# Optimization experiments

Measured on AMD Instinct MI355X. Metric: run time of the kernel, lower is better.

The kernel has to match this reference:

```python
import jax, jax.numpy as jnp
import numpy as np

N = 100000      # nodes
E = 1600000     # edges
D = 128         # hidden_dim
H = 8           # num_heads
DH = D // H     # per-head dim (out_dim in MultiHeadAttentionLayer)
EPS = 1e-5


def layer_norm(x, g, b):
    mu = jnp.mean(x, axis=-1, keepdims=True)
    var = jnp.var(x, axis=-1, keepdims=True)
    return (x - mu) * jax.lax.rsqrt(var + EPS) * g + b


def setup_inputs() -> dict:
    key = jax.random.key(0)
    ks = jax.random.split(key, 16)
    s = 1.0 / np.sqrt(D)
    inp = {
        "h": jax.random.normal(ks[0], (N, D), jnp.float32),
        "src": jax.random.randint(ks[1], (E,), 0, N, jnp.int32),
        "dst": jax.random.randint(ks[2], (E,), 0, N, jnp.int32),
        # attention projections (use_bias=False)
        "Wq": jax.random.uniform(ks[3], (D, D), jnp.float32, -s, s),
        "Wk": jax.random.uniform(ks[4], (D, D), jnp.float32, -s, s),
        "Wv": jax.random.uniform(ks[5], (D, D), jnp.float32, -s, s),
        # output projection O (bias=True)
        "Wo": jax.random.uniform(ks[6], (D, D), jnp.float32, -s, s),
        "bo": jnp.zeros((D,), jnp.float32),
        # layer norms
        "g1": jnp.ones((D,), jnp.float32),
        "b1": jnp.zeros((D,), jnp.float32),
        "g2": jnp.ones((D,), jnp.float32),
        "b2": jnp.zeros((D,), jnp.float32),
        # FFN
        "W1": jax.random.uniform(ks[7], (D, 2 * D), jnp.float32, -s, s),
        "c1": jnp.zeros((2 * D,), jnp.float32),
        "W2": jax.random.uniform(ks[8], (2 * D, D), jnp.float32, -1.0 / np.sqrt(2 * D), 1.0 / np.sqrt(2 * D)),
        "c2": jnp.zeros((D,), jnp.float32),
    }
    return inp


def reference(h, src, dst, Wq, Wk, Wv, Wo, bo, g1, b1, g2, b2, W1, c1, W2, c2):
    n = h.shape[0]
    Q = (h @ Wq).reshape(n, H, DH)
    K = (h @ Wk).reshape(n, H, DH)
    V = (h @ Wv).reshape(n, H, DH)

    # per-edge score: (K[src] * Q[dst]).sum(-1), scaled exp with clamp
    score = jnp.einsum('ehd,ehd->eh', K[src], Q[dst])          # [E, H]
    score = jnp.exp(jnp.clip(score / np.sqrt(DH), -5.0, 5.0))  # [E, H]

    # scatter-sum aggregation into destination nodes
    wV = jax.ops.segment_sum(V[src] * score[:, :, None], dst, num_segments=n)  # [N, H, DH]
    z = jax.ops.segment_sum(score, dst, num_segments=n)                        # [N, H]

    # possible_empty=True: divide only where z > 0
    zb = z[:, :, None]
    head_out = jnp.where(zb > 0, wV / jnp.where(zb > 0, zb, 1.0), wV)

    a = head_out.reshape(n, D) @ Wo + bo
    hh = layer_norm(h + a, g1, b1)
    ff = jax.nn.relu(hh @ W1 + c1) @ W2 + c2
    return layer_norm(hh + ff, g2, b2)
```

## Files before the change

### kernel.cpp

```cpp
#include <hip/hip_runtime.h>
#include <hip/hip_bf16.h>

#define D 128

typedef __attribute__((ext_vector_type(8))) short short8;
typedef __attribute__((ext_vector_type(4))) float float4v;
typedef __attribute__((ext_vector_type(2))) float float2v;

__device__ __forceinline__ float4v mfma16(short8 a, short8 b, float4v c) {
  return __builtin_amdgcn_mfma_f32_16x16x32_bf16(a, b, c, 0, 0, 0);
}
__device__ __forceinline__ float b2f(__hip_bfloat16 x) { return __bfloat162float(x); }
__device__ __forceinline__ __hip_bfloat16 f2b(float x) { return __float2bfloat16(x); }
__device__ __forceinline__ unsigned short f2b_bits(float x) {
  __hip_bfloat16 h = __float2bfloat16(x);
  return *reinterpret_cast<unsigned short*>(&h);
}

__device__ __forceinline__ float ldf(const float* p, size_t i) { return p[i]; }
__device__ __forceinline__ float ldf(const __hip_bfloat16* p, size_t i) { return b2f(p[i]); }
__device__ __forceinline__ void stf(float* p, size_t i, float v) { p[i] = v; }
__device__ __forceinline__ void stf(__hip_bfloat16* p, size_t i, float v) { p[i] = f2b(v); }

__device__ __forceinline__ void bar_lds() {
  asm volatile("s_waitcnt lgkmcnt(0)\n\ts_barrier" ::: "memory");
}

__device__ __forceinline__ float2v up2(unsigned w) {
  float2v r;
  r.x = __uint_as_float(w << 16);
  r.y = __uint_as_float(w & 0xffff0000u);
  return r;
}
__device__ __forceinline__ unsigned char f2fp8(float x) {
  int r = __builtin_amdgcn_cvt_pk_fp8_f32(x, x, 0, false);
  return (unsigned char)(r & 0xff);
}
__device__ __forceinline__ float2v cvt2lo(unsigned w) {
  return __builtin_amdgcn_cvt_pk_f32_fp8(w, false);
}
__device__ __forceinline__ float2v cvt2hi(unsigned w) {
  return __builtin_amdgcn_cvt_pk_f32_fp8(w, true);
}

__device__ __forceinline__ short8 cvt8(float4 u0, float4 u1) {
  short8 a;
  a[0] = (short)f2b_bits(u0.x); a[1] = (short)f2b_bits(u0.y);
  a[2] = (short)f2b_bits(u0.z); a[3] = (short)f2b_bits(u0.w);
  a[4] = (short)f2b_bits(u1.x); a[5] = (short)f2b_bits(u1.y);
  a[6] = (short)f2b_bits(u1.z); a[7] = (short)f2b_bits(u1.w);
  return a;
}

__global__ void k_cast_w(const float* __restrict__ wq, const float* __restrict__ wk,
                         const float* __restrict__ wv, const float* __restrict__ wo,
                         const float* __restrict__ w1, const float* __restrict__ w2,
                         __hip_bfloat16* __restrict__ oq, __hip_bfloat16* __restrict__ ok,
                         __hip_bfloat16* __restrict__ ov, __hip_bfloat16* __restrict__ oo,
                         __hip_bfloat16* __restrict__ o1, __hip_bfloat16* __restrict__ o2) {
  int i = blockIdx.x * 256 + threadIdx.x;
  if (i < 65536) {
    int m = i & 16383;
    int which = i >> 14;
    const float* s = (which == 0) ? wq : (which == 1) ? wk : (which == 2) ? wv : wo;
    __hip_bfloat16* o = (which == 0) ? oq : (which == 1) ? ok : (which == 2) ? ov : oo;
    int j = m & 7, t2 = m >> 3;
    int col = t2 & 127, cq = t2 >> 7;
    o[m] = f2b(s[((cq >> 2) * 32 + (cq & 3) * 8 + j) * 128 + col]);
  } else if (i < 98304) {
    int m = i - 65536;
    int j = m & 7, t2 = m >> 3;
    int col = t2 & 255, cq = t2 >> 8;
    o1[m] = f2b(w1[((cq >> 2) * 32 + (cq & 3) * 8 + j) * 256 + col]);
  } else {
    int m = i - 98304;
    int j = m & 7, t2 = m >> 3;
    int col = t2 & 127, cq = t2 >> 7;
    o2[m] = f2b(w2[((cq >> 2) * 32 + (cq & 3) * 8 + j) * 128 + col]);
  }
}

#define MAXB 512

__global__ void k_bhist(const int* __restrict__ dst, int* __restrict__ bh, int E) {
  __shared__ int cnt[MAXB];
  for (int i = threadIdx.x; i < MAXB; i += 256) cnt[i] = 0;
  __syncthreads();
  for (int e = blockIdx.x * 256 + threadIdx.x; e < E; e += gridDim.x * 256)
    atomicAdd(&cnt[dst[e] >> 8], 1);
  __syncthreads();
  for (int i = threadIdx.x; i < MAXB; i += 256)
    if (cnt[i]) atomicAdd(&bh[i], cnt[i]);
}

__global__ void k_bscan(const int* __restrict__ bh, int* __restrict__ bbase,
                        int* __restrict__ bcur, int B) {
  __shared__ int sd[MAXB];
  int t = threadIdx.x;
  int v = (t < B) ? bh[t] : 0;
  sd[t] = v;
  __syncthreads();
  for (int o = 1; o < MAXB; o <<= 1) {
    int x = (t >= o) ? sd[t - o] : 0;
    __syncthreads();
    sd[t] += x;
    __syncthreads();
  }
  if (t < B) {
    int e = sd[t] - v;
    bbase[t] = e;
    bcur[t] = e;
  }
}

__global__ __launch_bounds__(256) void k_bin(const int* __restrict__ src,
                                             const int* __restrict__ dst,
                                             int* __restrict__ bcur,
                                             uint2* __restrict__ binned, int E) {
  __shared__ int cnt[MAXB];
  __shared__ int base[MAXB];
  const int t = threadIdx.x;
  const int e0 = blockIdx.x * 4096;
  for (int i = t; i < MAXB; i += 256) cnt[i] = 0;
  __syncthreads();
  int myb[16], myr[16], ms[16], md[16];
#pragma unroll
  for (int j = 0; j < 16; ++j) {
    int e = e0 + j * 256 + t;
    if (e < E) {
      int d = dst[e];
      ms[j] = src[e];
      md[j] = d;
      int b = d >> 8;
      myb[j] = b;
      myr[j] = atomicAdd(&cnt[b], 1);
    } else {
      myb[j] = -1;
    }
  }
  __syncthreads();
  for (int i = t; i < MAXB; i += 256)
    base[i] = cnt[i] ? atomicAdd(&bcur[i], cnt[i]) : 0;
  __syncthreads();
#pragma unroll
  for (int j = 0; j < 16; ++j)
    if (myb[j] >= 0)
      binned[(size_t)base[myb[j]] + myr[j]] = make_uint2((unsigned)ms[j], (unsigned)md[j]);
}

__global__ __launch_bounds__(256) void k_fine(const uint2* __restrict__ binned,
                                              const int* __restrict__ bh,
                                              const int* __restrict__ bbase,
                                              int* __restrict__ deg,
                                              int* __restrict__ offs,
                                              int* __restrict__ csr, int N) {
  __shared__ int cnt[256];
  __shared__ int cur[256];
  __shared__ int sd[256];
  const int b = blockIdx.x, t = threadIdx.x;
  const int node0 = b << 8;
  cnt[t] = 0;
  __syncthreads();
  const int s0 = bbase[b], len = bh[b];
  for (int i = t; i < len; i += 256) atomicAdd(&cnt[binned[(size_t)s0 + i].y & 255], 1);
  __syncthreads();
  int v = cnt[t];
  sd[t] = v;
  __syncthreads();
  for (int o = 1; o < 256; o <<= 1) {
    int x = (t >= o) ? sd[t - o] : 0;
    __syncthreads();
    sd[t] += x;
    __syncthreads();
  }
  int excl = sd[t] - v;
  cur[t] = excl;
  int node = node0 + t;
  if (node < N) {
    deg[node] = v;
    offs[node] = s0 + excl;
  }
  __syncthreads();
  for (int i = t; i < len; i += 256) {
    uint2 ed = binned[(size_t)s0 + i];
    int p = atomicAdd(&cur[ed.y & 255], 1);
    csr[s0 + p] = (int)ed.x;
  }
}

__global__ __launch_bounds__(512) void gemm_qkv5(const float* __restrict__ A,
                                                 const uint4* __restrict__ wqF,
                                                 const uint4* __restrict__ wkF,
                                                 const uint4* __restrict__ wvF,
                                                 __hip_bfloat16* __restrict__ Q,
                                                 unsigned char* __restrict__ KV8,
                                                 int Nrow) {
  __shared__ short W[3 * 16384];
  const int t = threadIdx.x;
  {
    uint4* W4 = (uint4*)W;
    for (int i = t; i < 2048; i += 512) {
      W4[i] = wqF[i];
      W4[i + 2048] = wkF[i];
      W4[i + 4096] = wvF[i];
    }
  }
  __syncthreads();
  const int lane = t & 63;
  const int ct = t >> 6;
  const int n = lane & 15, quad = lane >> 4;
  const int fbase = quad * 128 + ct * 16 + n;
  const int ntiles = Nrow >> 4;
  const int koff = ct * 32 + ((n >> 3) << 4) + (n & 7);
  int rt = blockIdx.x;
  if (rt >= ntiles) return;
  float4 u[8];
  {
    const float* Ap = A + (size_t)(rt * 16 + n) * 128 + quad * 8;
#pragma unroll
    for (int c = 0; c < 4; ++c) {
      u[2 * c] = *(const float4*)(Ap + c * 32);
      u[2 * c + 1] = *(const float4*)(Ap + c * 32 + 4);
    }
  }
  while (true) {
    const int rtn = rt + gridDim.x;
    const bool more = rtn < ntiles;
    float4 un[8];
    if (more) {
      const float* Ap = A + (size_t)(rtn * 16 + n) * 128 + quad * 8;
#pragma unroll
      for (int c = 0; c < 4; ++c) {
        un[2 * c] = *(const float4*)(Ap + c * 32);
        un[2 * c + 1] = *(const float4*)(Ap + c * 32 + 4);
      }
    }
    short8 a[4];
#pragma unroll
    for (int c = 0; c < 4; ++c) a[c] = cvt8(u[2 * c], u[2 * c + 1]);
    float4v aq = {0.f, 0.f, 0.f, 0.f}, ak = aq, av = aq;
#pragma unroll
    for (int c = 0; c < 4; ++c) {
      const int fo = (fbase + c * 512) * 8;
      short8 fq = *(const short8*)&W[fo];
      short8 fk = *(const short8*)&W[16384 + fo];
      short8 fv = *(const short8*)&W[32768 + fo];
      aq = mfma16(a[c], fq, aq);
      ak = mfma16(a[c], fk, ak);
      av = mfma16(a[c], fv, av);
    }
#pragma unroll
    for (int r = 0; r < 4; ++r) {
      int grow = rt * 16 + quad * 4 + r;
      Q[(size_t)grow * 128 + ct * 16 + n] = f2b(aq[r]);
      size_t b = (size_t)grow * 256 + koff;
      KV8[b] = f2fp8(ak[r]);
      KV8[b + 8] = f2fp8(av[r]);
    }
    if (!more) break;
#pragma unroll
    for (int i = 0; i < 8; ++i) u[i] = un[i];
    rt = rtn;
  }
}

template <int K, typename TR, typename TO>
__global__ __launch_bounds__(512) void ln_gemm(const short* __restrict__ A,
                                               const uint4* __restrict__ BF4,
                                               const float* __restrict__ bias,
                                               const TR* __restrict__ resid,
                                               const float* __restrict__ gam,
                                               const float* __restrict__ bet,
                                               TO* __restrict__ Out, int Nrow) {
  __shared__ short W[K * 128];
  __shared__ float tile[16][132];
  const int t = threadIdx.x;
  {
    uint4* W4 = (uint4*)W;
    for (int i = t; i < K * 16; i += 512) W4[i] = BF4[i];
  }
  __syncthreads();
  const int lane = t & 63;
  const int ct = t >> 6;
  const int n = lane & 15, quad = lane >> 4;
  const int fbase = quad * 128 + ct * 16 + n;
  float biasv = bias[ct * 16 + n];
  const int row2 = t >> 5, sub = t & 31;
  float ga0 = gam[sub],      ga1 = gam[sub + 32];
  float ga2 = gam[sub + 64], ga3 = gam[sub + 96];
  float be0 = bet[sub],      be1 = bet[sub + 32];
  float be2 = bet[sub + 64], be3 = bet[sub + 96];
  const int ntiles = Nrow >> 4;
  for (int rt = blockIdx.x; rt < ntiles; rt += gridDim.x) {
    const short8* Ap = (const short8*)(A + (size_t)(rt * 16 + n) * K + quad * 8);
    short8 a[K / 32];
    float rs[4];
#pragma unroll
    for (int c = 0; c < K / 32; ++c) a[c] = Ap[c * 4];
#pragma unroll
    for (int r = 0; r < 4; ++r)
      rs[r] = ldf(resid, (size_t)(rt * 16 + quad * 4 + r) * 128 + ct * 16 + n);
    float4v acc = {0.f, 0.f, 0.f, 0.f};
#pragma unroll
    for (int c = 0; c < K / 32; ++c) {
      short8 bf = *(const short8*)&W[(fbase + c * 512) * 8];
      acc = mfma16(a[c], bf, acc);
    }
#pragma unroll
    for (int r = 0; r < 4; ++r)
      tile[quad * 4 + r][ct * 16 + n] = acc[r] + biasv + rs[r];
    bar_lds();
    float x0 = tile[row2][sub], x1 = tile[row2][sub + 32];
    float x2 = tile[row2][sub + 64], x3 = tile[row2][sub + 96];
    float s = x0 + x1 + x2 + x3;
    float s2 = x0 * x0 + x1 * x1 + x2 * x2 + x3 * x3;
#pragma unroll
    for (int o = 16; o >= 1; o >>= 1) {
      s += __shfl_xor(s, o);
      s2 += __shfl_xor(s2, o);
    }
    float mean = s * 0.0078125f;
    float var = s2 * 0.0078125f - mean * mean;
    float rstd = rsqrtf(var + 1e-5f);
    size_t base = (size_t)(rt * 16 + row2) * 128;
    stf(Out, base + sub,      (x0 - mean) * rstd * ga0 + be0);
    stf(Out, base + sub + 32, (x1 - mean) * rstd * ga1 + be1);
    stf(Out, base + sub + 64, (x2 - mean) * rstd * ga2 + be2);
    stf(Out, base + sub + 96, (x3 - mean) * rstd * ga3 + be3);
    bar_lds();
  }
}

__global__ __launch_bounds__(512) void ffn_ln(const short* __restrict__ hh,
                                              const uint4* __restrict__ W1F4,
                                              const float* __restrict__ c1,
                                              const uint4* __restrict__ W2F4,
                                              const float* __restrict__ c2,
                                              const float* __restrict__ gam,
                                              const float* __restrict__ bet,
                                              float* __restrict__ Out, int Nrow) {
  __shared__ short W1[32768];
  __shared__ short W2[32768];
  __shared__ short mid[16][264];
  __shared__ float tile[16][132];
  const int t = threadIdx.x;
  {
    uint4* a4 = (uint4*)W1;
    uint4* b4 = (uint4*)W2;
    for (int i = t; i < 4096; i += 512) {
      a4[i] = W1F4[i];
      b4[i] = W2F4[i];
    }
  }
  __syncthreads();
  const int lane = t & 63;
  const int wv = t >> 6;
  const int n = lane & 15, quad = lane >> 4;
  float b1v0 = c1[(wv * 2) * 16 + n], b1v1 = c1[(wv * 2 + 1) * 16 + n];
  float b2v = c2[wv * 16 + n];
  const int row2 = t >> 5, sub = t & 31;
  float ga0 = gam[sub],      ga1 = gam[sub + 32];
  float ga2 = gam[sub + 64], ga3 = gam[sub + 96];
  float be0 = bet[sub],      be1 = bet[sub + 32];
  float be2 = bet[sub + 64], be3 = bet[sub + 96];
  const int ntiles = Nrow >> 4;
  const __hip_bfloat16* hb = (const __hip_bfloat16*)hh;
  const int f1b0 = quad * 256 + (wv * 2) * 16 + n;
  const int f1b1 = quad * 256 + (wv * 2 + 1) * 16 + n;
  const int f2b = quad * 128 + wv * 16 + n;
  int rt = blockIdx.x;
  if (rt >= ntiles) return;
  short8 a[4];
  __hip_bfloat16 rs[4];
  {
    const short8* Ap = (const short8*)(hh + (size_t)(rt * 16 + n) * 128 + quad * 8);
#pragma unroll
    for (int c = 0; c < 4; ++c) a[c] = Ap[c * 4];
#pragma unroll
    for (int r = 0; r < 4; ++r)
      rs[r] = hb[(size_t)(rt * 16 + quad * 4 + r) * 128 + wv * 16 + n];
  }
  while (true) {
    const int rtn = rt + gridDim.x;
    const bool more = rtn < ntiles;
    short8 an[4];
    __hip_bfloat16 rsn[4];
    if (more) {
      const short8* Ap = (const short8*)(hh + (size_t)(rtn * 16 + n) * 128 + quad * 8);
#pragma unroll
      for (int c = 0; c < 4; ++c) an[c] = Ap[c * 4];
#pragma unroll
      for (int r = 0; r < 4; ++r)
        rsn[r] = hb[(size_t)(rtn * 16 + quad * 4 + r) * 128 + wv * 16 + n];
    }
    float4v a10 = {0.f, 0.f, 0.f, 0.f}, a11 = a10;
#pragma unroll
    for (int c = 0; c < 4; ++c) {
      short8 f1a = *(const short8*)&W1[(f1b0 + c * 1024) * 8];
      short8 f1c = *(const short8*)&W1[(f1b1 + c * 1024) * 8];
      a10 = mfma16(a[c], f1a, a10);
      a11 = mfma16(a[c], f1c, a11);
    }
#pragma unroll
    for (int r = 0; r < 4; ++r) {
      mid[quad * 4 + r][(wv * 2) * 16 + n] = (short)f2b_bits(fmaxf(a10[r] + b1v0, 0.f));
      mid[quad * 4 + r][(wv * 2 + 1) * 16 + n] = (short)f2b_bits(fmaxf(a11[r] + b1v1, 0.f));
    }
    bar_lds();
    float4v acc = {0.f, 0.f, 0.f, 0.f};
#pragma unroll
    for (int c = 0; c < 8; ++c) {
      short8 am = *(const short8*)&mid[n][quad * 8 + c * 32];
      short8 f2 = *(const short8*)&W2[(f2b + c * 512) * 8];
      acc = mfma16(am, f2, acc);
    }
#pragma unroll
    for (int r = 0; r < 4; ++r)
      tile[quad * 4 + r][wv * 16 + n] = acc[r] + b2v + b2f(rs[r]);
    bar_lds();
    float x0 = tile[row2][sub], x1 = tile[row2][sub + 32];
    float x2 = tile[row2][sub + 64], x3 = tile[row2][sub + 96];
    float s = x0 + x1 + x2 + x3;
    float s2 = x0 * x0 + x1 * x1 + x2 * x2 + x3 * x3;
#pragma unroll
    for (int o = 16; o >= 1; o >>= 1) {
      s += __shfl_xor(s, o);
      s2 += __shfl_xor(s2, o);
    }
    float mean = s * 0.0078125f;
    float var = s2 * 0.0078125f - mean * mean;
    float rstd = rsqrtf(var + 1e-5f);
    size_t base = (size_t)(rt * 16 + row2) * 128;
    Out[base + sub]      = (x0 - mean) * rstd * ga0 + be0;
    Out[base + sub + 32] = (x1 - mean) * rstd * ga1 + be1;
    Out[base + sub + 64] = (x2 - mean) * rstd * ga2 + be2;
    Out[base + sub + 96] = (x3 - mean) * rstd * ga3 + be3;
    bar_lds();
    if (!more) break;
#pragma unroll
    for (int c = 0; c < 4; ++c) a[c] = an[c];
#pragma unroll
    for (int r = 0; r < 4; ++r) rs[r] = rsn[r];
    rt = rtn;
  }
}

__global__ __launch_bounds__(256) void attn_agg5(const uint4* __restrict__ Q4,
                                                 const uint4* __restrict__ KV8,
                                                 const int* __restrict__ offs,
                                                 const int* __restrict__ deg,
                                                 const int* __restrict__ csr,
                                                 uint4* __restrict__ AT4, int N) {
  const int lane = threadIdx.x & 63;
  const int wv = threadIdx.x >> 6;
  const int e4 = lane >> 4;
  const int hd = (lane >> 1) & 7;
  const int hf = lane & 1;
  const int kvo = hd * 2 + hf;
  for (int node = blockIdx.x * 4 + wv; node < N; node += gridDim.x * 4) {
    uint4 qa = Q4[(size_t)node * 16 + kvo];
    float2v qv[4];
    qv[0] = up2(qa.x); qv[1] = up2(qa.y); qv[2] = up2(qa.z); qv[3] = up2(qa.w);
    float2v acc[4];
#pragma unroll
    for (int d = 0; d < 4; ++d) acc[d] = (float2v){0.f, 0.f};
    float z = 0.f;
    const int st = offs[node], dg = deg[node];
    if (dg > 0) {
      const int dgm1 = dg - 1;
      int s_cur = csr[st + min(e4, dgm1)];
      int s_nxt = (dg > 4) ? csr[st + min(4 + e4, dgm1)] : s_cur;
      uint4 ckv = KV8[(size_t)s_cur * 16 + kvo];
      int i = 0;
      while (true) {
        const bool more = (i + 4) < dg;
        uint4 nkv;
        int s_fut = s_nxt;
        if (more) {
          nkv = KV8[(size_t)s_nxt * 16 + kvo];
          s_fut = csr[st + min(i + 8 + e4, dgm1)];
        }
        float2v p2 = cvt2lo(ckv.x) * qv[0];
        p2 += cvt2hi(ckv.x) * qv[1];
        p2 += cvt2lo(ckv.y) * qv[2];
        p2 += cvt2hi(ckv.y) * qv[3];
        float p = p2.x + p2.y;
        p += __shfl_xor(p, 1);
        float sc = __expf(fminf(fmaxf(p * 0.25f, -5.f), 5.f));
        sc = ((i + e4) < dg) ? sc : 0.f;
        z += sc;
        float2v sv = {sc, sc};
        acc[0] += cvt2lo(ckv.z) * sv;
        acc[1] += cvt2hi(ckv.z) * sv;
        acc[2] += cvt2lo(ckv.w) * sv;
        acc[3] += cvt2hi(ckv.w) * sv;
        if (!more) break;
        ckv = nkv;
        s_nxt = s_fut;
        i += 4;
      }
    }
#pragma unroll
    for (int m = 16; m <= 32; m <<= 1) {
      z += __shfl_xor(z, m);
#pragma unroll
      for (int d = 0; d < 4; ++d) {
        acc[d].x += __shfl_xor(acc[d].x, m);
        acc[d].y += __shfl_xor(acc[d].y, m);
      }
    }
    if (e4 == 0) {
      float inv = (z > 0.f) ? 1.f / z : 1.f;
      unsigned r[4];
#pragma unroll
      for (int j = 0; j < 4; ++j)
        r[j] = (unsigned)f2b_bits(acc[j].x * inv) |
               ((unsigned)f2b_bits(acc[j].y * inv) << 16);
      AT4[(size_t)node * 16 + kvo] = make_uint4(r[0], r[1], r[2], r[3]);
    }
  }
}

extern "C" void kernel_launch(void* const* d_in, const int* in_sizes, int n_in,
                              void* d_out, int out_size, void* d_ws, size_t ws_size,
                              hipStream_t stream) {
  const float* h = (const float*)d_in[0];
  const int* src = (const int*)d_in[1];
  const int* dst = (const int*)d_in[2];
  const float* Wq = (const float*)d_in[3];
  const float* Wk = (const float*)d_in[4];
  const float* Wv = (const float*)d_in[5];
  const float* Wo = (const float*)d_in[6];
  const float* bo = (const float*)d_in[7];
  const float* g1 = (const float*)d_in[8];
  const float* b1 = (const float*)d_in[9];
  const float* g2 = (const float*)d_in[10];
  const float* b2 = (const float*)d_in[11];
  const float* W1 = (const float*)d_in[12];
  const float* c1 = (const float*)d_in[13];
  const float* W2 = (const float*)d_in[14];
  const float* c2 = (const float*)d_in[15];

  const int N = in_sizes[0] / D;
  const int E = in_sizes[1];
  const int B = (N + 255) >> 8;

  char* p = (char*)d_ws;
  auto carve = [&](size_t bytes) {
    char* r = p;
    p += (bytes + 255) & ~(size_t)255;
    return r;
  };
  short* ATb = (short*)carve((size_t)N * D * 2);
  short* Qb = (short*)carve((size_t)N * D * 2);
  unsigned char* KVb = (unsigned char*)carve((size_t)N * 256);
  short* wq = (short*)carve(16384 * 2);
  short* wk = (short*)carve(16384 * 2);
  short* wv = (short*)carve(16384 * 2);
  short* wo = (short*)carve(16384 * 2);
  short* w1 = (short*)carve(32768 * 2);
  short* w2 = (short*)carve(32768 * 2);
  int* deg = (int*)carve((size_t)N * 4);
  int* offs = (int*)carve((size_t)N * 4);
  int* bh = (int*)carve(MAXB * 4);
  int* bbase = (int*)carve(MAXB * 4);
  int* bcur = (int*)carve(MAXB * 4);
  uint2* binned = (uint2*)carve((size_t)E * 8);
  int* csr = (int*)carve((size_t)E * 4);
  short* hh = Qb;

  hipMemsetAsync(bh, 0, MAXB * 4, stream);
  k_bhist<<<1024, 256, 0, stream>>>(dst, bh, E);
  k_bscan<<<1, MAXB, 0, stream>>>(bh, bbase, bcur, B);
  k_bin<<<(E + 4095) / 4096, 256, 0, stream>>>(src, dst, bcur, binned, E);
  k_fine<<<B, 256, 0, stream>>>(binned, bh, bbase, deg, offs, csr, N);

  k_cast_w<<<512, 256, 0, stream>>>(Wq, Wk, Wv, Wo, W1, W2,
                                    (__hip_bfloat16*)wq, (__hip_bfloat16*)wk,
                                    (__hip_bfloat16*)wv, (__hip_bfloat16*)wo,
                                    (__hip_bfloat16*)w1, (__hip_bfloat16*)w2);

  gemm_qkv5<<<256, 512, 0, stream>>>(h, (const uint4*)wq, (const uint4*)wk,
                                     (const uint4*)wv, (__hip_bfloat16*)Qb, KVb, N);

  attn_agg5<<<(N + 3) >> 2, 256, 0, stream>>>((const uint4*)Qb, (const uint4*)KVb,
                                              offs, deg, csr, (uint4*)ATb, N);

  ln_gemm<128, float, __hip_bfloat16><<<768, 512, 0, stream>>>(
      ATb, (const uint4*)wo, bo, h, g1, b1, (__hip_bfloat16*)hh, N);
  ffn_ln<<<256, 512, 0, stream>>>(hh, (const uint4*)w1, c1, (const uint4*)w2, c2,
                                  g2, b2, (float*)d_out, N);
}
```

Baseline: 398.1 us.

## Build CSR with global atomics scatter and double-buffer LDS tiles to drop barriers

Replaces the two-level bucket binning CSR build (histogram of 256-node bins, binning pass, per-bin fine sort) with a direct per-node degree histogram via global atomics, a three-kernel prefix scan, and an atomic scatter of source indices. This removes the intermediate 8-byte binned edge buffer and its extra read/write pass, but uses random global atomics over 100k nodes and produces nondeterministic edge order within a node. Separately, the LDS tiles in ln_gemm and ffn_ln are double-buffered so the trailing barrier at the end of each row-tile iteration can be removed, shortening the synchronisation per tile.

```diff
diff --git a/kernel.cpp b/kernel.cpp
--- a/kernel.cpp
+++ b/kernel.cpp
@@ -80,91 +80,35 @@
   }
 }
 
-#define MAXB 512
-
-__global__ void k_bhist(const int* __restrict__ dst, int* __restrict__ bh, int E) {
-  __shared__ int cnt[MAXB];
-  for (int i = threadIdx.x; i < MAXB; i += 256) cnt[i] = 0;
+__global__ void k_hist(const int* __restrict__ dst, int* __restrict__ deg, int E) {
+  for (int e = blockIdx.x * 256 + threadIdx.x; e < E; e += gridDim.x * 256)
+    atomicAdd(&deg[dst[e]], 1);
+}
+
+__global__ __launch_bounds__(512) void k_scan1(const int* __restrict__ deg,
+                                               int* __restrict__ bsum, int N) {
+  __shared__ int ws[8];
+  const int t = threadIdx.x;
+  int node = blockIdx.x * 512 + t;
+  int v = (node < N) ? deg[node] : 0;
+  int s = v;
+#pragma unroll
+  for (int o = 1; o <= 32; o <<= 1) s += __shfl_xor(s, o);
+  if ((t & 63) == 0) ws[t >> 6] = s;
   __syncthreads();
-  for (int e = blockIdx.x * 256 + threadIdx.x; e < E; e += gridDim.x * 256)
-    atomicAdd(&cnt[dst[e] >> 8], 1);
-  __syncthreads();
-  for (int i = threadIdx.x; i < MAXB; i += 256)
-    if (cnt[i]) atomicAdd(&bh[i], cnt[i]);
-}
-
-__global__ void k_bscan(const int* __restrict__ bh, int* __restrict__ bbase,
-                        int* __restrict__ bcur, int B) {
-  __shared__ int sd[MAXB];
-  int t = threadIdx.x;
-  int v = (t < B) ? bh[t] : 0;
-  sd[t] = v;
-  __syncthreads();
-  for (int o = 1; o < MAXB; o <<= 1) {
-    int x = (t >= o) ? sd[t - o] : 0;
-    __syncthreads();
-    sd[t] += x;
-    __syncthreads();
-  }
-  if (t < B) {
-    int e = sd[t] - v;
-    bbase[t] = e;
-    bcur[t] = e;
-  }
-}
-
-__global__ __launch_bounds__(256) void k_bin(const int* __restrict__ src,
-                                             const int* __restrict__ dst,
-                                             int* __restrict__ bcur,
-                                             uint2* __restrict__ binned, int E) {
-  __shared__ int cnt[MAXB];
-  __shared__ int base[MAXB];
+  if (t == 0) {
+    int tot = 0;
+#pragma unroll
+    for (int w = 0; w < 8; ++w) tot += ws[w];
+    bsum[blockIdx.x] = tot;
+  }
+}
+
+__global__ __launch_bounds__(256) void k_scan2(const int* __restrict__ bsum,
+                                               int* __restrict__ bbase, int nb) {
+  __shared__ int sd[256];
   const int t = threadIdx.x;
-  const int e0 = blockIdx.x * 4096;
-  for (int i = t; i < MAXB; i += 256) cnt[i] = 0;
-  __syncthreads();
-  int myb[16], myr[16], ms[16], md[16];
-#pragma unroll
-  for (int j = 0; j < 16; ++j) {
-    int e = e0 + j * 256 + t;
-    if (e < E) {
-      int d = dst[e];
-      ms[j] = src[e];
-      md[j] = d;
-      int b = d >> 8;
-      myb[j] = b;
-      myr[j] = atomicAdd(&cnt[b], 1);
-    } else {
-      myb[j] = -1;
-    }
-  }
-  __syncthreads();
-  for (int i = t; i < MAXB; i += 256)
-    base[i] = cnt[i] ? atomicAdd(&bcur[i], cnt[i]) : 0;
-  __syncthreads();
-#pragma unroll
-  for (int j = 0; j < 16; ++j)
-    if (myb[j] >= 0)
-      binned[(size_t)base[myb[j]] + myr[j]] = make_uint2((unsigned)ms[j], (unsigned)md[j]);
-}
-
-__global__ __launch_bounds__(256) void k_fine(const uint2* __restrict__ binned,
-                                              const int* __restrict__ bh,
-                                              const int* __restrict__ bbase,
-                                              int* __restrict__ deg,
-                                              int* __restrict__ offs,
-                                              int* __restrict__ csr, int N) {
-  __shared__ int cnt[256];
-  __shared__ int cur[256];
-  __shared__ int sd[256];
-  const int b = blockIdx.x, t = threadIdx.x;
-  const int node0 = b << 8;
-  cnt[t] = 0;
-  __syncthreads();
-  const int s0 = bbase[b], len = bh[b];
-  for (int i = t; i < len; i += 256) atomicAdd(&cnt[binned[(size_t)s0 + i].y & 255], 1);
-  __syncthreads();
-  int v = cnt[t];
+  int v = (t < nb) ? bsum[t] : 0;
   sd[t] = v;
   __syncthreads();
   for (int o = 1; o < 256; o <<= 1) {
@@ -173,18 +117,38 @@
     sd[t] += x;
     __syncthreads();
   }
-  int excl = sd[t] - v;
-  cur[t] = excl;
-  int node = node0 + t;
+  if (t < nb) bbase[t] = sd[t] - v;
+}
+
+__global__ __launch_bounds__(512) void k_scan3(const int* __restrict__ deg,
+                                               const int* __restrict__ bbase,
+                                               int* __restrict__ offs,
+                                               int* __restrict__ cur, int N) {
+  __shared__ int sd[512];
+  const int t = threadIdx.x;
+  int node = blockIdx.x * 512 + t;
+  int v = (node < N) ? deg[node] : 0;
+  sd[t] = v;
+  __syncthreads();
+  for (int o = 1; o < 512; o <<= 1) {
+    int x = (t >= o) ? sd[t - o] : 0;
+    __syncthreads();
+    sd[t] += x;
+    __syncthreads();
+  }
   if (node < N) {
-    deg[node] = v;
-    offs[node] = s0 + excl;
-  }
-  __syncthreads();
-  for (int i = t; i < len; i += 256) {
-    uint2 ed = binned[(size_t)s0 + i];
-    int p = atomicAdd(&cur[ed.y & 255], 1);
-    csr[s0 + p] = (int)ed.x;
+    int e = bbase[blockIdx.x] + sd[t] - v;
+    offs[node] = e;
+    cur[node] = e;
+  }
+}
+
+__global__ void k_scatter(const int* __restrict__ src, const int* __restrict__ dst,
+                          int* __restrict__ cur, int* __restrict__ csr, int E) {
+  for (int e = blockIdx.x * 256 + threadIdx.x; e < E; e += gridDim.x * 256) {
+    int d = dst[e];
+    int p = atomicAdd(&cur[d], 1);
+    csr[p] = src[e];
   }
 }
 
@@ -273,7 +237,7 @@
                                                const float* __restrict__ bet,
                                                TO* __restrict__ Out, int Nrow) {
   __shared__ short W[K * 128];
-  __shared__ float tile[16][132];
+  __shared__ float tile[2][16][132];
   const int t = threadIdx.x;
   {
     uint4* W4 = (uint4*)W;
@@ -291,7 +255,8 @@
   float be0 = bet[sub],      be1 = bet[sub + 32];
   float be2 = bet[sub + 64], be3 = bet[sub + 96];
   const int ntiles = Nrow >> 4;
-  for (int rt = blockIdx.x; rt < ntiles; rt += gridDim.x) {
+  int pp = 0;
+  for (int rt = blockIdx.x; rt < ntiles; rt += gridDim.x, pp ^= 1) {
     const short8* Ap = (const short8*)(A + (size_t)(rt * 16 + n) * K + quad * 8);
     short8 a[K / 32];
     float rs[4];
@@ -308,10 +273,10 @@
     }
 #pragma unroll
     for (int r = 0; r < 4; ++r)
-      tile[quad * 4 + r][ct * 16 + n] = acc[r] + biasv + rs[r];
+      tile[pp][quad * 4 + r][ct * 16 + n] = acc[r] + biasv + rs[r];
     bar_lds();
-    float x0 = tile[row2][sub], x1 = tile[row2][sub + 32];
-    float x2 = tile[row2][sub + 64], x3 = tile[row2][sub + 96];
+    float x0 = tile[pp][row2][sub], x1 = tile[pp][row2][sub + 32];
+    float x2 = tile[pp][row2][sub + 64], x3 = tile[pp][row2][sub + 96];
     float s = x0 + x1 + x2 + x3;
     float s2 = x0 * x0 + x1 * x1 + x2 * x2 + x3 * x3;
 #pragma unroll
@@ -327,7 +292,6 @@
     stf(Out, base + sub + 32, (x1 - mean) * rstd * ga1 + be1);
     stf(Out, base + sub + 64, (x2 - mean) * rstd * ga2 + be2);
     stf(Out, base + sub + 96, (x3 - mean) * rstd * ga3 + be3);
-    bar_lds();
   }
 }
 
@@ -341,7 +305,7 @@
                                               float* __restrict__ Out, int Nrow) {
   __shared__ short W1[32768];
   __shared__ short W2[32768];
-  __shared__ short mid[16][264];
+  __shared__ short mid[2][16][264];
   __shared__ float tile[16][132];
   const int t = threadIdx.x;
   {
@@ -380,6 +344,7 @@
     for (int r = 0; r < 4; ++r)
       rs[r] = hb[(size_t)(rt * 16 + quad * 4 + r) * 128 + wv * 16 + n];
   }
+  int mp = 0;
   while (true) {
     const int rtn = rt + gridDim.x;
     const bool more = rtn < ntiles;
@@ -403,14 +368,14 @@
     }
 #pragma unroll
     for (int r = 0; r < 4; ++r) {
-      mid[quad * 4 + r][(wv * 2) * 16 + n] = (short)f2b_bits(fmaxf(a10[r] + b1v0, 0.f));
-      mid[quad * 4 + r][(wv * 2 + 1) * 16 + n] = (short)f2b_bits(fmaxf(a11[r] + b1v1, 0.f));
+      mid[mp][quad * 4 + r][(wv * 2) * 16 + n] = (short)f2b_bits(fmaxf(a10[r] + b1v0, 0.f));
+      mid[mp][quad * 4 + r][(wv * 2 + 1) * 16 + n] = (short)f2b_bits(fmaxf(a11[r] + b1v1, 0.f));
     }
     bar_lds();
     float4v acc = {0.f, 0.f, 0.f, 0.f};
 #pragma unroll
     for (int c = 0; c < 8; ++c) {
-      short8 am = *(const short8*)&mid[n][quad * 8 + c * 32];
+      short8 am = *(const short8*)&mid[mp][n][quad * 8 + c * 32];
       short8 f2 = *(const short8*)&W2[(f2b + c * 512) * 8];
       acc = mfma16(am, f2, acc);
     }
@@ -435,13 +400,13 @@
     Out[base + sub + 32] = (x1 - mean) * rstd * ga1 + be1;
     Out[base + sub + 64] = (x2 - mean) * rstd * ga2 + be2;
     Out[base + sub + 96] = (x3 - mean) * rstd * ga3 + be3;
-    bar_lds();
     if (!more) break;
 #pragma unroll
     for (int c = 0; c < 4; ++c) a[c] = an[c];
 #pragma unroll
     for (int r = 0; r < 4; ++r) rs[r] = rsn[r];
     rt = rtn;
+    mp ^= 1;
   }
 }
 
@@ -543,7 +508,7 @@
 
   const int N = in_sizes[0] / D;
   const int E = in_sizes[1];
-  const int B = (N + 255) >> 8;
+  const int NB = (N + 511) >> 9;
 
   char* p = (char*)d_ws;
   auto carve = [&](size_t bytes) {
@@ -562,18 +527,18 @@
   short* w2 = (short*)carve(32768 * 2);
   int* deg = (int*)carve((size_t)N * 4);
   int* offs = (int*)carve((size_t)N * 4);
-  int* bh = (int*)carve(MAXB * 4);
-  int* bbase = (int*)carve(MAXB * 4);
-  int* bcur = (int*)carve(MAXB * 4);
-  uint2* binned = (uint2*)carve((size_t)E * 8);
+  int* cur = (int*)carve((size_t)N * 4);
+  int* bsum = (int*)carve(256 * 4);
+  int* bbase = (int*)carve(256 * 4);
   int* csr = (int*)carve((size_t)E * 4);
   short* hh = Qb;
 
-  hipMemsetAsync(bh, 0, MAXB * 4, stream);
-  k_bhist<<<1024, 256, 0, stream>>>(dst, bh, E);
-  k_bscan<<<1, MAXB, 0, stream>>>(bh, bbase, bcur, B);
-  k_bin<<<(E + 4095) / 4096, 256, 0, stream>>>(src, dst, bcur, binned, E);
-  k_fine<<<B, 256, 0, stream>>>(binned, bh, bbase, deg, offs, csr, N);
+  hipMemsetAsync(deg, 0, (size_t)N * 4, stream);
+  k_hist<<<2048, 256, 0, stream>>>(dst, deg, E);
+  k_scan1<<<NB, 512, 0, stream>>>(deg, bsum, N);
+  k_scan2<<<1, 256, 0, stream>>>(bsum, bbase, NB);
+  k_scan3<<<NB, 512, 0, stream>>>(deg, bbase, offs, cur, N);
+  k_scatter<<<2048, 256, 0, stream>>>(src, dst, cur, csr, E);
 
   k_cast_w<<<512, 256, 0, stream>>>(Wq, Wk, Wv, Wo, W1, W2,
                                     (__hip_bfloat16*)wq, (__hip_bfloat16*)wk,
```

Result: slower. 534.5 us (+34.3%).

## Fuse graph CSR build and weight cast into one cooperative kernel, double-buffer LDS

Applied to the files above, without the earlier changes.

Merges the memset, bucket histogram, scan, binning, fine CSR sort and weight bf16 cast into a single cooperative kernel separated by grid.sync(). This removes several launches and the inter-kernel gaps between them. Binned edges are packed into one 32-bit word (src<<8 | dst&255), which halves the scatter buffer traffic but assumes node ids fit in 24 bits and that 512 blocks cover all edges. The LDS staging tiles in ln_gemm and ffn_ln are double-buffered so the trailing per-tile barrier can be dropped.

```diff
diff --git a/kernel.cpp b/kernel.cpp
--- a/kernel.cpp
+++ b/kernel.cpp
@@ -1,7 +1,11 @@
 #include <hip/hip_runtime.h>
 #include <hip/hip_bf16.h>
+#include <hip/hip_cooperative_groups.h>
+
+namespace cg = cooperative_groups;
 
 #define D 128
+#define MAXB 512
 
 typedef __attribute__((ext_vector_type(8))) short short8;
 typedef __attribute__((ext_vector_type(4))) float float4v;
@@ -52,139 +56,141 @@
   return a;
 }
 
-__global__ void k_cast_w(const float* __restrict__ wq, const float* __restrict__ wk,
-                         const float* __restrict__ wv, const float* __restrict__ wo,
-                         const float* __restrict__ w1, const float* __restrict__ w2,
-                         __hip_bfloat16* __restrict__ oq, __hip_bfloat16* __restrict__ ok,
-                         __hip_bfloat16* __restrict__ ov, __hip_bfloat16* __restrict__ oo,
-                         __hip_bfloat16* __restrict__ o1, __hip_bfloat16* __restrict__ o2) {
-  int i = blockIdx.x * 256 + threadIdx.x;
-  if (i < 65536) {
-    int m = i & 16383;
-    int which = i >> 14;
-    const float* s = (which == 0) ? wq : (which == 1) ? wk : (which == 2) ? wv : wo;
-    __hip_bfloat16* o = (which == 0) ? oq : (which == 1) ? ok : (which == 2) ? ov : oo;
-    int j = m & 7, t2 = m >> 3;
-    int col = t2 & 127, cq = t2 >> 7;
-    o[m] = f2b(s[((cq >> 2) * 32 + (cq & 3) * 8 + j) * 128 + col]);
-  } else if (i < 98304) {
-    int m = i - 65536;
-    int j = m & 7, t2 = m >> 3;
-    int col = t2 & 255, cq = t2 >> 8;
-    o1[m] = f2b(w1[((cq >> 2) * 32 + (cq & 3) * 8 + j) * 256 + col]);
-  } else {
-    int m = i - 98304;
-    int j = m & 7, t2 = m >> 3;
-    int col = t2 & 127, cq = t2 >> 7;
-    o2[m] = f2b(w2[((cq >> 2) * 32 + (cq & 3) * 8 + j) * 128 + col]);
-  }
-}
-
-#define MAXB 512
-
-__global__ void k_bhist(const int* __restrict__ dst, int* __restrict__ bh, int E) {
-  __shared__ int cnt[MAXB];
-  for (int i = threadIdx.x; i < MAXB; i += 256) cnt[i] = 0;
-  __syncthreads();
-  for (int e = blockIdx.x * 256 + threadIdx.x; e < E; e += gridDim.x * 256)
-    atomicAdd(&cnt[dst[e] >> 8], 1);
-  __syncthreads();
-  for (int i = threadIdx.x; i < MAXB; i += 256)
-    if (cnt[i]) atomicAdd(&bh[i], cnt[i]);
-}
-
-__global__ void k_bscan(const int* __restrict__ bh, int* __restrict__ bbase,
-                        int* __restrict__ bcur, int B) {
-  __shared__ int sd[MAXB];
-  int t = threadIdx.x;
-  int v = (t < B) ? bh[t] : 0;
-  sd[t] = v;
-  __syncthreads();
-  for (int o = 1; o < MAXB; o <<= 1) {
-    int x = (t >= o) ? sd[t - o] : 0;
-    __syncthreads();
-    sd[t] += x;
-    __syncthreads();
-  }
-  if (t < B) {
-    int e = sd[t] - v;
-    bbase[t] = e;
-    bcur[t] = e;
-  }
-}
-
-__global__ __launch_bounds__(256) void k_bin(const int* __restrict__ src,
-                                             const int* __restrict__ dst,
-                                             int* __restrict__ bcur,
-                                             uint2* __restrict__ binned, int E) {
-  __shared__ int cnt[MAXB];
-  __shared__ int base[MAXB];
-  const int t = threadIdx.x;
-  const int e0 = blockIdx.x * 4096;
-  for (int i = t; i < MAXB; i += 256) cnt[i] = 0;
-  __syncthreads();
-  int myb[16], myr[16], ms[16], md[16];
-#pragma unroll
-  for (int j = 0; j < 16; ++j) {
-    int e = e0 + j * 256 + t;
-    if (e < E) {
-      int d = dst[e];
-      ms[j] = src[e];
-      md[j] = d;
-      int b = d >> 8;
-      myb[j] = b;
-      myr[j] = atomicAdd(&cnt[b], 1);
+__global__ __launch_bounds__(256) void k_prep(
+    const int* __restrict__ src, const int* __restrict__ dst,
+    int* __restrict__ bh, int* __restrict__ bbase, int* __restrict__ bcur,
+    unsigned* __restrict__ binned, int* __restrict__ deg, int* __restrict__ offs,
+    int* __restrict__ csr,
+    const float* __restrict__ wq, const float* __restrict__ wk,
+    const float* __restrict__ wv, const float* __restrict__ wo,
+    const float* __restrict__ w1, const float* __restrict__ w2,
+    __hip_bfloat16* __restrict__ oq, __hip_bfloat16* __restrict__ ok,
+    __hip_bfloat16* __restrict__ ov, __hip_bfloat16* __restrict__ oo,
+    __hip_bfloat16* __restrict__ o1, __hip_bfloat16* __restrict__ o2,
+    int N, int E, int NBuck) {
+  __shared__ int smem[1024];
+  cg::grid_group grid = cg::this_grid();
+  const int t = threadIdx.x, b = blockIdx.x;
+  const int gthreads = gridDim.x * 256;
+  const int gid = b * 256 + t;
+
+  for (int i = gid; i < MAXB; i += gthreads) bh[i] = 0;
+  grid.sync();
+
+  {
+    for (int i = t; i < MAXB; i += 256) smem[i] = 0;
+    __syncthreads();
+    for (int e = gid; e < E; e += gthreads) atomicAdd(&smem[dst[e] >> 8], 1);
+    __syncthreads();
+    for (int i = t; i < MAXB; i += 256)
+      if (smem[i]) atomicAdd(&bh[i], smem[i]);
+  }
+  {
+    int i = gid;
+    if (i < 65536) {
+      int m = i & 16383;
+      int which = i >> 14;
+      const float* s = (which == 0) ? wq : (which == 1) ? wk : (which == 2) ? wv : wo;
+      __hip_bfloat16* o = (which == 0) ? oq : (which == 1) ? ok : (which == 2) ? ov : oo;
+      int j = m & 7, t2 = m >> 3;
+      int col = t2 & 127, cq = t2 >> 7;
+      o[m] = f2b(s[((cq >> 2) * 32 + (cq & 3) * 8 + j) * 128 + col]);
+    } else if (i < 98304) {
+      int m = i - 65536;
+      int j = m & 7, t2 = m >> 3;
+      int col = t2 & 255, cq = t2 >> 8;
+      o1[m] = f2b(w1[((cq >> 2) * 32 + (cq & 3) * 8 + j) * 256 + col]);
     } else {
-      myb[j] = -1;
-    }
-  }
-  __syncthreads();
-  for (int i = t; i < MAXB; i += 256)
-    base[i] = cnt[i] ? atomicAdd(&bcur[i], cnt[i]) : 0;
-  __syncthreads();
-#pragma unroll
-  for (int j = 0; j < 16; ++j)
-    if (myb[j] >= 0)
-      binned[(size_t)base[myb[j]] + myr[j]] = make_uint2((unsigned)ms[j], (unsigned)md[j]);
-}
-
-__global__ __launch_bounds__(256) void k_fine(const uint2* __restrict__ binned,
-                                              const int* __restrict__ bh,
-                                              const int* __restrict__ bbase,
-                                              int* __restrict__ deg,
-                                              int* __restrict__ offs,
-                                              int* __restrict__ csr, int N) {
-  __shared__ int cnt[256];
-  __shared__ int cur[256];
-  __shared__ int sd[256];
-  const int b = blockIdx.x, t = threadIdx.x;
-  const int node0 = b << 8;
-  cnt[t] = 0;
-  __syncthreads();
-  const int s0 = bbase[b], len = bh[b];
-  for (int i = t; i < len; i += 256) atomicAdd(&cnt[binned[(size_t)s0 + i].y & 255], 1);
-  __syncthreads();
-  int v = cnt[t];
-  sd[t] = v;
-  __syncthreads();
-  for (int o = 1; o < 256; o <<= 1) {
-    int x = (t >= o) ? sd[t - o] : 0;
-    __syncthreads();
-    sd[t] += x;
-    __syncthreads();
-  }
-  int excl = sd[t] - v;
-  cur[t] = excl;
-  int node = node0 + t;
-  if (node < N) {
-    deg[node] = v;
-    offs[node] = s0 + excl;
-  }
-  __syncthreads();
-  for (int i = t; i < len; i += 256) {
-    uint2 ed = binned[(size_t)s0 + i];
-    int p = atomicAdd(&cur[ed.y & 255], 1);
-    csr[s0 + p] = (int)ed.x;
+      int m = i - 98304;
+      int j = m & 7, t2 = m >> 3;
+      int col = t2 & 127, cq = t2 >> 7;
+      o2[m] = f2b(w2[((cq >> 2) * 32 + (cq & 3) * 8 + j) * 128 + col]);
+    }
+  }
+  grid.sync();
+
+  if (b == 0) {
+    int v0 = bh[2 * t], v1 = bh[2 * t + 1];
+    int pair = v0 + v1;
+    smem[t] = pair;
+    __syncthreads();
+    for (int o = 1; o < 256; o <<= 1) {
+      int x = (t >= o) ? smem[t - o] : 0;
+      __syncthreads();
+      smem[t] += x;
+      __syncthreads();
+    }
+    int ep = smem[t] - pair;
+    bbase[2 * t] = ep;
+    bcur[2 * t] = ep;
+    bbase[2 * t + 1] = ep + v0;
+    bcur[2 * t + 1] = ep + v0;
+  }
+  grid.sync();
+
+  {
+    int* cnt = smem;
+    int* base = smem + 512;
+    for (int i = t; i < MAXB; i += 256) cnt[i] = 0;
+    __syncthreads();
+    int myb[16], myr[16];
+    unsigned pk[16];
+    const int e0 = b * 4096;
+#pragma unroll
+    for (int j = 0; j < 16; ++j) {
+      int e = e0 + j * 256 + t;
+      if (e < E) {
+        int d = dst[e];
+        pk[j] = ((unsigned)src[e] << 8) | (unsigned)(d & 255);
+        int bk = d >> 8;
+        myb[j] = bk;
+        myr[j] = atomicAdd(&cnt[bk], 1);
+      } else {
+        myb[j] = -1;
+      }
+    }
+    __syncthreads();
+    for (int i = t; i < MAXB; i += 256)
+      base[i] = cnt[i] ? atomicAdd(&bcur[i], cnt[i]) : 0;
+    __syncthreads();
+#pragma unroll
+    for (int j = 0; j < 16; ++j)
+      if (myb[j] >= 0) binned[(size_t)base[myb[j]] + myr[j]] = pk[j];
+  }
+  grid.sync();
+
+  if (b < NBuck) {
+    int* cnt = smem;
+    int* cur = smem + 256;
+    int* sd = smem + 512;
+    const int node0 = b << 8;
+    cnt[t] = 0;
+    __syncthreads();
+    const int s0 = bbase[b], len = bh[b];
+    for (int i = t; i < len; i += 256) atomicAdd(&cnt[binned[(size_t)s0 + i] & 255], 1);
+    __syncthreads();
+    int v = cnt[t];
+    sd[t] = v;
+    __syncthreads();
+    for (int o = 1; o < 256; o <<= 1) {
+      int x = (t >= o) ? sd[t - o] : 0;
+      __syncthreads();
+      sd[t] += x;
+      __syncthreads();
+    }
+    int excl = sd[t] - v;
+    cur[t] = excl;
+    int node = node0 + t;
+    if (node < N) {
+      deg[node] = v;
+      offs[node] = s0 + excl;
+    }
+    __syncthreads();
+    for (int i = t; i < len; i += 256) {
+      unsigned ed = binned[(size_t)s0 + i];
+      int p = atomicAdd(&cur[ed & 255], 1);
+      csr[s0 + p] = (int)(ed >> 8);
+    }
   }
 }
 
@@ -273,7 +279,7 @@
                                                const float* __restrict__ bet,
                                                TO* __restrict__ Out, int Nrow) {
   __shared__ short W[K * 128];
-  __shared__ float tile[16][132];
+  __shared__ float tile[2][16][132];
   const int t = threadIdx.x;
   {
     uint4* W4 = (uint4*)W;
@@ -291,7 +297,8 @@
   float be0 = bet[sub],      be1 = bet[sub + 32];
   float be2 = bet[sub + 64], be3 = bet[sub + 96];
   const int ntiles = Nrow >> 4;
-  for (int rt = blockIdx.x; rt < ntiles; rt += gridDim.x) {
+  int pp = 0;
+  for (int rt = blockIdx.x; rt < ntiles; rt += gridDim.x, pp ^= 1) {
     const short8* Ap = (const short8*)(A + (size_t)(rt * 16 + n) * K + quad * 8);
     short8 a[K / 32];
     float rs[4];
@@ -308,10 +315,10 @@
     }
 #pragma unroll
     for (int r = 0; r < 4; ++r)
-      tile[quad * 4 + r][ct * 16 + n] = acc[r] + biasv + rs[r];
+      tile[pp][quad * 4 + r][ct * 16 + n] = acc[r] + biasv + rs[r];
     bar_lds();
-    float x0 = tile[row2][sub], x1 = tile[row2][sub + 32];
-    float x2 = tile[row2][sub + 64], x3 = tile[row2][sub + 96];
+    float x0 = tile[pp][row2][sub], x1 = tile[pp][row2][sub + 32];
+    float x2 = tile[pp][row2][sub + 64], x3 = tile[pp][row2][sub + 96];
     float s = x0 + x1 + x2 + x3;
     float s2 = x0 * x0 + x1 * x1 + x2 * x2 + x3 * x3;
 #pragma unroll
@@ -327,7 +334,6 @@
     stf(Out, base + sub + 32, (x1 - mean) * rstd * ga1 + be1);
     stf(Out, base + sub + 64, (x2 - mean) * rstd * ga2 + be2);
     stf(Out, base + sub + 96, (x3 - mean) * rstd * ga3 + be3);
-    bar_lds();
   }
 }
 
@@ -341,7 +347,7 @@
                                               float* __restrict__ Out, int Nrow) {
   __shared__ short W1[32768];
   __shared__ short W2[32768];
-  __shared__ short mid[16][264];
+  __shared__ short mid[2][16][264];
   __shared__ float tile[16][132];
   const int t = threadIdx.x;
   {
@@ -380,6 +386,7 @@
     for (int r = 0; r < 4; ++r)
       rs[r] = hb[(size_t)(rt * 16 + quad * 4 + r) * 128 + wv * 16 + n];
   }
+  int mp = 0;
   while (true) {
     const int rtn = rt + gridDim.x;
     const bool more = rtn < ntiles;
@@ -403,14 +410,14 @@
     }
 #pragma unroll
     for (int r = 0; r < 4; ++r) {
-      mid[quad * 4 + r][(wv * 2) * 16 + n] = (short)f2b_bits(fmaxf(a10[r] + b1v0, 0.f));
-      mid[quad * 4 + r][(wv * 2 + 1) * 16 + n] = (short)f2b_bits(fmaxf(a11[r] + b1v1, 0.f));
+      mid[mp][quad * 4 + r][(wv * 2) * 16 + n] = (short)f2b_bits(fmaxf(a10[r] + b1v0, 0.f));
+      mid[mp][quad * 4 + r][(wv * 2 + 1) * 16 + n] = (short)f2b_bits(fmaxf(a11[r] + b1v1, 0.f));
     }
     bar_lds();
     float4v acc = {0.f, 0.f, 0.f, 0.f};
 #pragma unroll
     for (int c = 0; c < 8; ++c) {
-      short8 am = *(const short8*)&mid[n][quad * 8 + c * 32];
+      short8 am = *(const short8*)&mid[mp][n][quad * 8 + c * 32];
       short8 f2 = *(const short8*)&W2[(f2b + c * 512) * 8];
       acc = mfma16(am, f2, acc);
     }
@@ -435,13 +442,13 @@
     Out[base + sub + 32] = (x1 - mean) * rstd * ga1 + be1;
     Out[base + sub + 64] = (x2 - mean) * rstd * ga2 + be2;
     Out[base + sub + 96] = (x3 - mean) * rstd * ga3 + be3;
-    bar_lds();
     if (!more) break;
 #pragma unroll
     for (int c = 0; c < 4; ++c) a[c] = an[c];
 #pragma unroll
     for (int r = 0; r < 4; ++r) rs[r] = rsn[r];
     rt = rtn;
+    mp ^= 1;
   }
 }
 
@@ -541,9 +548,9 @@
   const float* W2 = (const float*)d_in[14];
   const float* c2 = (const float*)d_in[15];
 
-  const int N = in_sizes[0] / D;
-  const int E = in_sizes[1];
-  const int B = (N + 255) >> 8;
+  int N = in_sizes[0] / D;
+  int E = in_sizes[1];
+  int NBuck = (N + 255) >> 8;
 
   char* p = (char*)d_ws;
   auto carve = [&](size_t bytes) {
@@ -565,20 +572,23 @@
   int* bh = (int*)carve(MAXB * 4);
   int* bbase = (int*)carve(MAXB * 4);
   int* bcur = (int*)carve(MAXB * 4);
-  uint2* binned = (uint2*)carve((size_t)E * 8);
+  unsigned* binned = (unsigned*)carve((size_t)E * 4);
   int* csr = (int*)carve((size_t)E * 4);
   short* hh = Qb;
 
-  hipMemsetAsync(bh, 0, MAXB * 4, stream);
-  k_bhist<<<1024, 256, 0, stream>>>(dst, bh, E);
-  k_bscan<<<1, MAXB, 0, stream>>>(bh, bbase, bcur, B);
-  k_bin<<<(E + 4095) / 4096, 256, 0, stream>>>(src, dst, bcur, binned, E);
-  k_fine<<<B, 256, 0, stream>>>(binned, bh, bbase, deg, offs, csr, N);
-
-  k_cast_w<<<512, 256, 0, stream>>>(Wq, Wk, Wv, Wo, W1, W2,
-                                    (__hip_bfloat16*)wq, (__hip_bfloat16*)wk,
-                                    (__hip_bfloat16*)wv, (__hip_bfloat16*)wo,
-                                    (__hip_bfloat16*)w1, (__hip_bfloat16*)w2);
+  __hip_bfloat16* oq = (__hip_bfloat16*)wq;
+  __hip_bfloat16* ok = (__hip_bfloat16*)wk;
+  __hip_bfloat16* ov = (__hip_bfloat16*)wv;
+  __hip_bfloat16* oo = (__hip_bfloat16*)wo;
+  __hip_bfloat16* o1 = (__hip_bfloat16*)w1;
+  __hip_bfloat16* o2 = (__hip_bfloat16*)w2;
+
+  void* args[] = {(void*)&src, (void*)&dst, (void*)&bh, (void*)&bbase, (void*)&bcur,
+                  (void*)&binned, (void*)&deg, (void*)&offs, (void*)&csr,
+                  (void*)&Wq, (void*)&Wk, (void*)&Wv, (void*)&Wo, (void*)&W1, (void*)&W2,
+                  (void*)&oq, (void*)&ok, (void*)&ov, (void*)&oo, (void*)&o1, (void*)&o2,
+                  (void*)&N, (void*)&E, (void*)&NBuck};
+  hipLaunchCooperativeKernel((const void*)k_prep, dim3(512), dim3(256), args, 0, stream);
 
   gemm_qkv5<<<256, 512, 0, stream>>>(h, (const uint4*)wq, (const uint4*)wk,
                                      (const uint4*)wv, (__hip_bfloat16*)Qb, KVb, N);
```

Result: slower. 623.4 us (+56.6%).
